# Kernel tuning notes

Measured on AMD Instinct MI355X. Metric: run time of the kernel, lower is better.

The kernel has to match this reference:

```python
import jax, jax.numpy as jnp
import numpy as np

N_GRAPHS = 256      # graphs in the batch
N_PER = 52          # nodes per peptide graph (module default num_nodes=52)
IN_CH = 21          # amino-acid one-hot features
HIDDEN = 128
OUT_EG = 128
LATENT = 64
N_LAYERS = 4


def _fc_edges(n_graphs, n_per):
    """Block-diagonal fully-connected directed edges (no self loops)."""
    base = np.arange(n_per)
    r, c = np.meshgrid(base, base, indexing='ij')
    mask = r != c
    r, c = r[mask], c[mask]                       # [n_per*(n_per-1)]
    offs = (np.arange(n_graphs) * n_per)[:, None]
    row = (r[None, :] + offs).reshape(-1)
    col = (c[None, :] + offs).reshape(-1)
    return row.astype(np.int32), col.astype(np.int32)


def setup_inputs() -> dict:
    key = jax.random.key(0)
    ks = iter(jax.random.split(key, 40))

    def rn(shape, scale=0.05):
        return jax.random.normal(next(ks), shape, dtype=jnp.float32) * scale

    N = N_GRAPHS * N_PER
    row, col = _fc_edges(N_GRAPHS, N_PER)
    L, H = N_LAYERS, HIDDEN
    return {
        'x': jax.random.normal(next(ks), (N, IN_CH), dtype=jnp.float32),
        'pos': jax.random.normal(next(ks), (N, 3), dtype=jnp.float32),
        'edge_row': jnp.asarray(row),
        'edge_col': jnp.asarray(col),
        'batch': jnp.repeat(jnp.arange(N_GRAPHS, dtype=jnp.int32), N_PER),
        'emb_in_w': rn((IN_CH, H)), 'emb_in_b': jnp.zeros((H,), jnp.float32),
        'edge_w1': rn((L, 2 * H + 1, H)), 'edge_b1': jnp.zeros((L, H), jnp.float32),
        'edge_w2': rn((L, H, H)), 'edge_b2': jnp.zeros((L, H), jnp.float32),
        'node_w1': rn((L, 2 * H, H)), 'node_b1': jnp.zeros((L, H), jnp.float32),
        'node_w2': rn((L, H, H)), 'node_b2': jnp.zeros((L, H), jnp.float32),
        'coord_w1': rn((L, H, H)), 'coord_b1': jnp.zeros((L, H), jnp.float32),
        'coord_w2': rn((L, H, 1), scale=0.001),   # xavier gain=0.001, no bias
        'emb_out_w': rn((H, OUT_EG)), 'emb_out_b': jnp.zeros((OUT_EG,), jnp.float32),
        'mean_w': rn((OUT_EG, LATENT)), 'mean_b': jnp.zeros((LATENT,), jnp.float32),
        'logvar_w': rn((OUT_EG, LATENT)), 'logvar_b': jnp.zeros((LATENT,), jnp.float32),
    }


def _segment_mean(data, ids, n):
    s = jax.ops.segment_sum(data, ids, num_segments=n)
    cnt = jax.ops.segment_sum(jnp.ones((data.shape[0],), data.dtype), ids, num_segments=n)
    return s / jnp.clip(cnt, 1.0)[:, None]


def _egcl(h, coord, row, col, p):
    """One E_GCL layer (residual=True, coords_agg='mean', no attention/tanh/normalize)."""
    ew1, eb1, ew2, eb2, nw1, nb1, nw2, nb2, cw1, cb1, cw2 = p
    n = h.shape[0]
    coord_diff = coord[row] - coord[col]                     # [E,3]
    radial = jnp.sum(coord_diff * coord_diff, axis=1, keepdims=True)  # [E,1]
    # edge model
    m = jnp.concatenate([h[row], h[col], radial], axis=1)    # [E,2H+1]
    m = jax.nn.silu(m @ ew1 + eb1)
    edge_feat = jax.nn.silu(m @ ew2 + eb2)                   # [E,H]
    # coord model: per-edge scalar, mean-aggregated onto source nodes
    t = jax.nn.silu(edge_feat @ cw1 + cb1) @ cw2             # [E,1]
    coord = coord + _segment_mean(coord_diff * t, row, n)
    # node model: sum-aggregate edge features, MLP, residual
    agg = jax.ops.segment_sum(edge_feat, row, num_segments=n)
    z = jnp.concatenate([h, agg], axis=1)                    # [N,2H]
    z = jax.nn.silu(z @ nw1 + nb1)
    h = h + (z @ nw2 + nb2)
    return h, coord


def reference(x, pos, edge_row, edge_col, batch,
              emb_in_w, emb_in_b,
              edge_w1, edge_b1, edge_w2, edge_b2,
              node_w1, node_b1, node_w2, node_b2,
              coord_w1, coord_b1, coord_w2,
              emb_out_w, emb_out_b,
              mean_w, mean_b, logvar_w, logvar_b):
    h = x @ emb_in_w + emb_in_b
    coord = pos
    for i in range(edge_w1.shape[0]):
        h, coord = _egcl(h, coord, edge_row, edge_col,
                         (edge_w1[i], edge_b1[i], edge_w2[i], edge_b2[i],
                          node_w1[i], node_b1[i], node_w2[i], node_b2[i],
                          coord_w1[i], coord_b1[i], coord_w2[i]))
    h = h @ emb_out_w + emb_out_b                            # embedding_out
    g = _segment_mean(h, batch, N_GRAPHS)                    # global_mean_pool
    mean = g @ mean_w + mean_b
    log_var = g @ logvar_w + logvar_b
    return mean, log_var
```

## Files before the change

kernel.cpp:

```cpp
#include <hip/hip_runtime.h>

constexpr int NPER = 52;
constexpr int HID  = 128;
constexpr int INCH = 21;
constexpr int NLAY = 4;
constexpr int LATD = 64;
constexpr int NGRAPH = 256;
constexpr int TPB  = 1024;
constexpr int TSTR = 424;
constexpr int TILE = 16 * TSTR;

typedef short short8 __attribute__((ext_vector_type(8)));
typedef float f32x4  __attribute__((ext_vector_type(4)));

constexpr int W1T_OFF = 0;
constexpr int W1T_SZ  = NLAY * 256 * HID;
constexpr int W2T_OFF = W1T_OFF + W1T_SZ;
constexpr int W2T_SZ  = NLAY * HID * HID;
constexpr int C1T_OFF = W2T_OFF + W2T_SZ;
constexpr int C1T_SZ  = NLAY * HID * HID;
constexpr int N1T_OFF = C1T_OFF + C1T_SZ;
constexpr int N1T_SZ  = NLAY * HID * 2 * HID;
constexpr int N2T_OFF = N1T_OFF + N1T_SZ;
constexpr int N2T_SZ  = NLAY * HID * HID;
constexpr int WS_ELEMS = N2T_OFF + N2T_SZ;

__device__ __forceinline__ unsigned cvt_pk_bf16(float a, float b) {
    unsigned r;
    asm("v_cvt_pk_bf16_f32 %0, %1, %2" : "=v"(r) : "v"(a), "v"(b));
    return r;
}
__device__ __forceinline__ unsigned short f2bf(float f) {
    return (unsigned short)cvt_pk_bf16(f, f);
}
__device__ __forceinline__ float bf2f(unsigned short h) {
    return __uint_as_float(((unsigned)h) << 16);
}
__device__ __forceinline__ float fast_rcp(float x) {
    float r;
    asm("v_rcp_f32 %0, %1" : "=v"(r) : "v"(x));
    return r;
}
__device__ __forceinline__ float silu_f(float v) {
    return v * fast_rcp(1.0f + __expf(-v));
}
__device__ __forceinline__ f32x4 mfma16(short8 a, short8 b, f32x4 c) {
    return __builtin_amdgcn_mfma_f32_16x16x32_bf16(a, b, c, 0, 0, 0);
}

__device__ __forceinline__ int tidx(int row, int e) {
    return (e >> 3) * TSTR + row * 8 + (e & 7);
}

__global__ void conv_w(const float* __restrict__ ew1, const float* __restrict__ ew2,
                       const float* __restrict__ cw1, const float* __restrict__ nw1,
                       const float* __restrict__ nw2, unsigned short* __restrict__ ws)
{
    int idx = blockIdx.x * 256 + threadIdx.x;
    if (idx >= WS_ELEMS) return;
    float v;
    if (idx < W2T_OFF) {
        int t = idx - W1T_OFF;
        int L = t / (256 * HID), rem = t % (256 * HID);
        int n = rem / HID, k = rem % HID;
        v = (n < HID) ? ew1[(size_t)L * 257 * HID + k * HID + n]
                      : ew1[(size_t)L * 257 * HID + (HID + k) * HID + (n - HID)];
    } else if (idx < C1T_OFF) {
        int t = idx - W2T_OFF;
        int L = t / (HID * HID), rem = t % (HID * HID);
        int n = rem / HID, k = rem % HID;
        v = ew2[(size_t)L * HID * HID + k * HID + n];
    } else if (idx < N1T_OFF) {
        int t = idx - C1T_OFF;
        int L = t / (HID * HID), rem = t % (HID * HID);
        int n = rem / HID, k = rem % HID;
        v = cw1[(size_t)L * HID * HID + k * HID + n];
    } else if (idx < N2T_OFF) {
        int t = idx - N1T_OFF;
        int L = t / (HID * 2 * HID), rem = t % (HID * 2 * HID);
        int n = rem / (2 * HID), k = rem % (2 * HID);
        v = nw1[(size_t)L * 2 * HID * HID + k * HID + n];
    } else {
        int t = idx - N2T_OFF;
        int L = t / (HID * HID), rem = t % (HID * HID);
        int n = rem / HID, k = rem % HID;
        v = nw2[(size_t)L * HID * HID + k * HID + n];
    }
    ws[idx] = f2bf(v);
}

constexpr int LDS_FLOATS = 1024 + 156 + 156 + 128 + 512 + 128;
constexpr size_t SHMEM_BYTES = (size_t)8 * TILE * 2 + LDS_FLOATS * 4;

__device__ __forceinline__ void coord_agg(int r, int rr, const float* tpart,
                                          const float* coord_s, float* cacc_s, int lane)
{
    float dx = 0.f, dy = 0.f, dz = 0.f;
    if (lane < NPER) {
        const float* tb = tpart + rr * 256;
        float tc = tb[lane] + tb[64 + lane] + tb[128 + lane] + tb[192 + lane];
        dx = (coord_s[r * 3 + 0] - coord_s[lane * 3 + 0]) * tc;
        dy = (coord_s[r * 3 + 1] - coord_s[lane * 3 + 1]) * tc;
        dz = (coord_s[r * 3 + 2] - coord_s[lane * 3 + 2]) * tc;
    }
    #pragma unroll
    for (int m = 1; m < 64; m <<= 1) {
        dx += __shfl_xor(dx, m); dy += __shfl_xor(dy, m); dz += __shfl_xor(dz, m);
    }
    if (lane == 0) {
        cacc_s[r * 3 + 0] = dx; cacc_s[r * 3 + 1] = dy; cacc_s[r * 3 + 2] = dz;
    }
}

extern "C" __global__ void __launch_bounds__(TPB)
egnn_mfma(const float* __restrict__ x, const float* __restrict__ pos,
          const float* __restrict__ emb_in_w, const float* __restrict__ emb_in_b,
          const float* __restrict__ edge_w1,
          const float* __restrict__ edge_b1, const float* __restrict__ edge_b2,
          const float* __restrict__ node_b1, const float* __restrict__ node_b2,
          const float* __restrict__ coord_b1, const float* __restrict__ coord_w2,
          const float* __restrict__ emb_out_w, const float* __restrict__ emb_out_b,
          const float* __restrict__ mean_w, const float* __restrict__ mean_b,
          const float* __restrict__ logvar_w, const float* __restrict__ logvar_b,
          const unsigned short* __restrict__ ws, float* __restrict__ out)
{
    extern __shared__ __align__(16) char smem[];
    unsigned short* m0_t = (unsigned short*)smem;
    unsigned short* m1_t = m0_t + TILE;
    unsigned short* e0_t = m1_t + TILE;
    unsigned short* e1_t = e0_t + TILE;
    unsigned short* h_t  = e1_t + TILE;
    unsigned short* ag_t = h_t  + TILE;
    unsigned short* A_t  = ag_t + TILE;
    unsigned short* B_t  = A_t  + TILE;
    float* aggp    = (float*)(B_t + TILE);
    float* coord_s = aggp + 1024;
    float* cacc_s  = coord_s + 156;
    float* rad_s   = cacc_s + 156;
    float* tpart   = rad_s + 128;
    float* wr_s    = tpart + 512;

    const int g    = blockIdx.x;
    const int tid  = threadIdx.x;
    const int lane = tid & 63;
    const int wv   = tid >> 6;
    const int mp   = wv >> 2;
    const int np   = wv & 3;
    const int l15  = lane & 15;
    const int kb   = lane >> 4;
    const int rowA = mp * 16 + l15;
    const int crow0 = mp * 16 + kb * 4;
    const int n0   = 32 * np + l15;
    const int n1   = n0 + 16;
    const int jp   = 2 * lane;
    const int pb   = (jp >> 3) * TSTR + (jp & 7);
    const int fo   = kb * TSTR + rowA * 8;

    {
        float* xs = (float*)m0_t;
        for (int p = tid; p < NPER * INCH; p += TPB) xs[p] = x[(size_t)g * NPER * INCH + p];
        for (int p = tid; p < NPER * 3; p += TPB)    coord_s[p] = pos[(size_t)g * NPER * 3 + p];
    }
    __syncthreads();

    for (int p = tid; p < NPER * HID; p += TPB) {
        int c = p >> 7, j = p & 127;
        float s = emb_in_b[j];
        #pragma unroll 7
        for (int k = 0; k < INCH; ++k) s += ((float*)m0_t)[c * INCH + k] * emb_in_w[k * HID + j];
        h_t[tidx(c, j)] = f2bf(s);
    }
    __syncthreads();

    for (int L = 0; L < NLAY; ++L) {
        const unsigned short* w1t = ws + W1T_OFF + (size_t)L * 256 * HID;
        const unsigned short* w2t = ws + W2T_OFF + (size_t)L * HID * HID;
        const unsigned short* c1t = ws + C1T_OFF + (size_t)L * HID * HID;
        const unsigned short* n1t = ws + N1T_OFF + (size_t)L * HID * 2 * HID;
        const unsigned short* n2t = ws + N2T_OFF + (size_t)L * HID * HID;

        short8 wE[8], wC[8];
        #pragma unroll
        for (int s = 0; s < 4; ++s) {
            wE[s]     = *(const short8*)(w2t + (size_t)n0 * HID + 32 * s + 8 * kb);
            wE[4 + s] = *(const short8*)(w2t + (size_t)n1 * HID + 32 * s + 8 * kb);
            wC[s]     = *(const short8*)(c1t + (size_t)n0 * HID + 32 * s + 8 * kb);
            wC[4 + s] = *(const short8*)(c1t + (size_t)n1 * HID + 32 * s + 8 * kb);
        }
        float eb2v[2], cb1v[2], cw2v[2];
        eb2v[0] = edge_b2[L * HID + n0];  eb2v[1] = edge_b2[L * HID + n1];
        cb1v[0] = coord_b1[L * HID + n0]; cb1v[1] = coord_b1[L * HID + n1];
        cw2v[0] = coord_w2[L * HID + n0]; cw2v[1] = coord_w2[L * HID + n1];
        if (tid < HID) wr_s[tid] = edge_w1[(size_t)L * 257 * HID + 256 * HID + tid];

        {
            f32x4 acc[4];
            #pragma unroll
            for (int q = 0; q < 4; ++q) acc[q] = (f32x4){0.f, 0.f, 0.f, 0.f};
            #pragma unroll
            for (int s = 0; s < 4; ++s) {
                short8 af = *(const short8*)(h_t + fo + s * 4 * TSTR);
                #pragma unroll
                for (int q = 0; q < 4; ++q) {
                    int n = l15 + 16 * (4 * np + q);
                    short8 bf = *(const short8*)(w1t + (size_t)n * HID + 32 * s + 8 * kb);
                    acc[q] = mfma16(af, bf, acc[q]);
                }
            }
            #pragma unroll
            for (int q = 0; q < 4; ++q) {
                int n = l15 + 16 * (4 * np + q);
                float eb1 = (n < HID) ? edge_b1[L * HID + n] : 0.f;
                #pragma unroll
                for (int reg = 0; reg < 4; ++reg) {
                    int c = crow0 + reg;
                    if (c < NPER) {
                        float v = acc[q][reg] + eb1;
                        if (n < HID) A_t[tidx(c, n)] = f2bf(v);
                        else         B_t[tidx(c, n - HID)] = f2bf(v);
                    }
                }
            }
        }
        if (tid < NPER) {
            float dx = coord_s[0] - coord_s[tid * 3 + 0];
            float dy = coord_s[1] - coord_s[tid * 3 + 1];
            float dz = coord_s[2] - coord_s[tid * 3 + 2];
            rad_s[tid] = dx * dx + dy * dy + dz * dz;
        } else if (tid >= 64 && tid < 64 + NPER) {
            int c = tid - 64;
            float dx = coord_s[3] - coord_s[c * 3 + 0];
            float dy = coord_s[4] - coord_s[c * 3 + 1];
            float dz = coord_s[5] - coord_s[c * 3 + 2];
            rad_s[64 + c] = dx * dx + dy * dy + dz * dz;
        }
        __syncthreads();

        const float wrl = wr_s[jp], wrh = wr_s[jp + 1];

        for (int gp = 0; gp < 26; ++gp) {
            const int r0 = 2 * gp, r1 = r0 + 1;

            {
                unsigned pa0 = *(const unsigned*)(A_t + pb + r0 * 8);
                unsigned pa1 = *(const unsigned*)(A_t + pb + r1 * 8);
                float A0l = bf2f((unsigned short)(pa0 & 0xffff)), A0h = bf2f((unsigned short)(pa0 >> 16));
                float A1l = bf2f((unsigned short)(pa1 & 0xffff)), A1h = bf2f((unsigned short)(pa1 >> 16));
                for (int j = wv; j < 2 * NPER; j += 16) {
                    int rr = (j >= NPER);
                    int c  = rr ? j - NPER : j;
                    float Al = rr ? A1l : A0l, Ah = rr ? A1h : A0h;
                    float rad = rad_s[rr * 64 + c];
                    unsigned bp = *(const unsigned*)(B_t + pb + c * 8);
                    float v0 = Al + bf2f((unsigned short)(bp & 0xffff)) + rad * wrl;
                    float v1 = Ah + bf2f((unsigned short)(bp >> 16))    + rad * wrh;
                    unsigned mv = cvt_pk_bf16(silu_f(v0), silu_f(v1));
                    *(unsigned*)((rr ? m1_t : m0_t) + pb + c * 8) = mv;
                }
            }
            __syncthreads();

            {
                f32x4 e00 = (f32x4){0.f,0.f,0.f,0.f}, e01 = e00, e10 = e00, e11 = e00;
                #pragma unroll
                for (int s = 0; s < 4; ++s) {
                    short8 af0 = *(const short8*)(m0_t + fo + s * 4 * TSTR);
                    short8 af1 = *(const short8*)(m1_t + fo + s * 4 * TSTR);
                    e00 = mfma16(af0, wE[s], e00); e01 = mfma16(af0, wE[4 + s], e01);
                    e10 = mfma16(af1, wE[s], e10); e11 = mfma16(af1, wE[4 + s], e11);
                }
                #pragma unroll
                for (int rr = 0; rr < 2; ++rr) {
                    f32x4 ea = rr ? e10 : e00, eb = rr ? e11 : e01;
                    unsigned short* et = rr ? e1_t : e0_t;
                    const int r = rr ? r1 : r0;
                    float a0 = 0.f, a1 = 0.f;
                    #pragma unroll
                    for (int reg = 0; reg < 4; ++reg) {
                        int c = crow0 + reg;
                        float v0 = silu_f(ea[reg] + eb2v[0]);
                        float v1 = silu_f(eb[reg] + eb2v[1]);
                        if (c < NPER) {
                            et[tidx(c, n0)] = f2bf(v0);
                            et[tidx(c, n1)] = f2bf(v1);
                            if (c != r) { a0 += v0; a1 += v1; }
                        }
                    }
                    a0 += __shfl_xor(a0, 16); a0 += __shfl_xor(a0, 32);
                    a1 += __shfl_xor(a1, 16); a1 += __shfl_xor(a1, 32);
                    if (kb == 0) {
                        float* ar = aggp + (rr * 4 + mp) * HID;
                        ar[n0] = a0; ar[n1] = a1;
                    }
                }
                if (wv < 2 && gp > 0) coord_agg(2 * gp - 2 + wv, wv, tpart, coord_s, cacc_s, lane);
            }
            __syncthreads();

            {
                f32x4 y00 = (f32x4){0.f,0.f,0.f,0.f}, y01 = y00, y10 = y00, y11 = y00;
                #pragma unroll
                for (int s = 0; s < 4; ++s) {
                    short8 af0 = *(const short8*)(e0_t + fo + s * 4 * TSTR);
                    short8 af1 = *(const short8*)(e1_t + fo + s * 4 * TSTR);
                    y00 = mfma16(af0, wC[s], y00); y01 = mfma16(af0, wC[4 + s], y01);
                    y10 = mfma16(af1, wC[s], y10); y11 = mfma16(af1, wC[4 + s], y11);
                }
                #pragma unroll
                for (int rr = 0; rr < 2; ++rr) {
                    f32x4 ya = rr ? y10 : y00, yb = rr ? y11 : y01;
                    float* tp = tpart + (rr * 4 + np) * 64;
                    #pragma unroll
                    for (int reg = 0; reg < 4; ++reg) {
                        float v = silu_f(ya[reg] + cb1v[0]) * cw2v[0]
                                + silu_f(yb[reg] + cb1v[1]) * cw2v[1];
                        v += __shfl_xor(v, 1); v += __shfl_xor(v, 2);
                        v += __shfl_xor(v, 4); v += __shfl_xor(v, 8);
                        if (l15 == 0) tp[crow0 + reg] = v;
                    }
                }
            }
            if (tid < 256) {
                int rr = tid >> 7, t = tid & 127;
                const float* ap = aggp + rr * 512;
                float a = ap[t] + ap[128 + t] + ap[256 + t] + ap[384 + t];
                ag_t[tidx(2 * gp + rr, t)] = f2bf(a);
            } else if (tid < 384 && gp + 1 < 26) {
                int t = tid - 256, rr = t >> 6, c = t & 63;
                if (c < NPER) {
                    int r = 2 * (gp + 1) + rr;
                    float dx = coord_s[r * 3 + 0] - coord_s[c * 3 + 0];
                    float dy = coord_s[r * 3 + 1] - coord_s[c * 3 + 1];
                    float dz = coord_s[r * 3 + 2] - coord_s[c * 3 + 2];
                    rad_s[rr * 64 + c] = dx * dx + dy * dy + dz * dz;
                }
            }
            __syncthreads();
        }

        if (wv < 2) coord_agg(50 + wv, wv, tpart, coord_s, cacc_s, lane);
        {
            float nb1v[2];
            nb1v[0] = node_b1[L * HID + n0]; nb1v[1] = node_b1[L * HID + n1];
            f32x4 z0 = (f32x4){0.f,0.f,0.f,0.f}, z1 = z0;
            #pragma unroll
            for (int s = 0; s < 4; ++s) {
                short8 af = *(const short8*)(h_t + fo + s * 4 * TSTR);
                z0 = mfma16(af, *(const short8*)(n1t + (size_t)n0 * 2 * HID + 32 * s + 8 * kb), z0);
                z1 = mfma16(af, *(const short8*)(n1t + (size_t)n1 * 2 * HID + 32 * s + 8 * kb), z1);
            }
            #pragma unroll
            for (int s = 0; s < 4; ++s) {
                short8 af = *(const short8*)(ag_t + fo + s * 4 * TSTR);
                z0 = mfma16(af, *(const short8*)(n1t + (size_t)n0 * 2 * HID + HID + 32 * s + 8 * kb), z0);
                z1 = mfma16(af, *(const short8*)(n1t + (size_t)n1 * 2 * HID + HID + 32 * s + 8 * kb), z1);
            }
            #pragma unroll
            for (int reg = 0; reg < 4; ++reg) {
                int c = crow0 + reg;
                if (c < NPER) {
                    m0_t[tidx(c, n0)] = f2bf(silu_f(z0[reg] + nb1v[0]));
                    m0_t[tidx(c, n1)] = f2bf(silu_f(z1[reg] + nb1v[1]));
                }
            }
        }
        __syncthreads();

        if (tid < NPER * 3) coord_s[tid] += cacc_s[tid] * (1.0f / 51.0f);
        {
            float nb2v[2];
            nb2v[0] = node_b2[L * HID + n0]; nb2v[1] = node_b2[L * HID + n1];
            f32x4 d0 = (f32x4){0.f,0.f,0.f,0.f}, d1 = d0;
            #pragma unroll
            for (int s = 0; s < 4; ++s) {
                short8 af = *(const short8*)(m0_t + fo + s * 4 * TSTR);
                d0 = mfma16(af, *(const short8*)(n2t + (size_t)n0 * HID + 32 * s + 8 * kb), d0);
                d1 = mfma16(af, *(const short8*)(n2t + (size_t)n1 * HID + 32 * s + 8 * kb), d1);
            }
            #pragma unroll
            for (int reg = 0; reg < 4; ++reg) {
                int c = crow0 + reg;
                if (c < NPER) {
                    int i0 = tidx(c, n0), i1 = tidx(c, n1);
                    h_t[i0] = f2bf(bf2f(h_t[i0]) + d0[reg] + nb2v[0]);
                    h_t[i1] = f2bf(bf2f(h_t[i1]) + d1[reg] + nb2v[1]);
                }
            }
        }
        __syncthreads();
    }

    float* gm = aggp;
    float* eg = aggp + HID;
    if (tid < HID) {
        float s = 0.f;
        for (int c = 0; c < NPER; ++c) s += bf2f(h_t[tidx(c, tid)]);
        gm[tid] = s * (1.0f / 52.0f);
    }
    __syncthreads();
    if (tid < HID) {
        float s = emb_out_b[tid];
        #pragma unroll 4
        for (int k = 0; k < HID; ++k) s += gm[k] * emb_out_w[k * HID + tid];
        eg[tid] = s;
    }
    __syncthreads();
    if (tid < 2 * LATD) {
        const int  l   = tid & (LATD - 1);
        const bool ism = tid < LATD;
        const float* W = ism ? mean_w : logvar_w;
        float s = ism ? mean_b[l] : logvar_b[l];
        #pragma unroll 4
        for (int k = 0; k < HID; ++k) s += eg[k] * W[k * LATD + l];
        out[(ism ? 0 : NGRAPH * LATD) + g * LATD + l] = s;
    }
}

extern "C" void kernel_launch(void* const* d_in, const int* in_sizes, int n_in,
                              void* d_out, int out_size, void* d_ws, size_t ws_size,
                              hipStream_t stream) {
    const float* x         = (const float*)d_in[0];
    const float* pos       = (const float*)d_in[1];
    const float* emb_in_w  = (const float*)d_in[5];
    const float* emb_in_b  = (const float*)d_in[6];
    const float* edge_w1   = (const float*)d_in[7];
    const float* edge_b1   = (const float*)d_in[8];
    const float* edge_w2   = (const float*)d_in[9];
    const float* edge_b2   = (const float*)d_in[10];
    const float* node_w1   = (const float*)d_in[11];
    const float* node_b1   = (const float*)d_in[12];
    const float* node_w2   = (const float*)d_in[13];
    const float* node_b2   = (const float*)d_in[14];
    const float* coord_w1  = (const float*)d_in[15];
    const float* coord_b1  = (const float*)d_in[16];
    const float* coord_w2  = (const float*)d_in[17];
    const float* emb_out_w = (const float*)d_in[18];
    const float* emb_out_b = (const float*)d_in[19];
    const float* mean_w    = (const float*)d_in[20];
    const float* mean_b    = (const float*)d_in[21];
    const float* logvar_w  = (const float*)d_in[22];
    const float* logvar_b  = (const float*)d_in[23];

    unsigned short* ws = (unsigned short*)d_ws;

    conv_w<<<(WS_ELEMS + 255) / 256, 256, 0, stream>>>(edge_w1, edge_w2, coord_w1,
                                                       node_w1, node_w2, ws);

    (void)hipFuncSetAttribute(reinterpret_cast<const void*>(egnn_mfma),
                              hipFuncAttributeMaxDynamicSharedMemorySize,
                              (int)SHMEM_BYTES);

    hipLaunchKernelGGL(egnn_mfma, dim3(NGRAPH), dim3(TPB), SHMEM_BYTES, stream,
                       x, pos, emb_in_w, emb_in_b, edge_w1,
                       edge_b1, edge_b2, node_b1, node_b2,
                       coord_b1, coord_w2, emb_out_w, emb_out_b,
                       mean_w, mean_b, logvar_w, logvar_b,
                       ws, (float*)d_out);
}
```

Before: 805.7 us.

## Split fused EGNN kernel into per-layer edge/node kernels with half-graph row splits

Replaces the single persistent per-graph kernel with separate launches: embedding, per-layer edge kernels split across two blocks per graph (26 rows each), per-layer node-update kernels, and a head kernel. Node features, aggregates and coordinates now round-trip through global workspace between launches. The goal is to double the block count (512 vs 256 blocks on a many-CU GPU) and cut LDS use for better occupancy, and it also reworks silu to use raw exp/rcp instructions. In exchange it adds launch overhead and extra global memory traffic.

Result: slower. 1.861 ms (+130.9%).

```diff
diff --git a/kernel.cpp b/kernel.cpp
--- a/kernel.cpp
+++ b/kernel.cpp
@@ -1,29 +1,29 @@
 #include <hip/hip_runtime.h>
 
-constexpr int NPER = 52;
-constexpr int HID  = 128;
-constexpr int INCH = 21;
-constexpr int NLAY = 4;
-constexpr int LATD = 64;
-constexpr int NGRAPH = 256;
+constexpr int NPER = 52, HID = 128, INCH = 21, NLAY = 4, LATD = 64, NGRAPH = 256;
 constexpr int TPB  = 1024;
 constexpr int TSTR = 424;
 constexpr int TILE = 16 * TSTR;
+constexpr int ASTR = 216;
+constexpr int ATILE = 16 * ASTR;
+constexpr int GSTR = 512;
+constexpr int GTILE = 16 * GSTR;
+constexpr int RHALF = 26;
+constexpr int CSTR = 160;
 
 typedef short short8 __attribute__((ext_vector_type(8)));
 typedef float f32x4  __attribute__((ext_vector_type(4)));
 
-constexpr int W1T_OFF = 0;
-constexpr int W1T_SZ  = NLAY * 256 * HID;
-constexpr int W2T_OFF = W1T_OFF + W1T_SZ;
-constexpr int W2T_SZ  = NLAY * HID * HID;
-constexpr int C1T_OFF = W2T_OFF + W2T_SZ;
-constexpr int C1T_SZ  = NLAY * HID * HID;
-constexpr int N1T_OFF = C1T_OFF + C1T_SZ;
-constexpr int N1T_SZ  = NLAY * HID * 2 * HID;
-constexpr int N2T_OFF = N1T_OFF + N1T_SZ;
-constexpr int N2T_SZ  = NLAY * HID * HID;
+constexpr int W1T_OFF = 0,                 W1T_SZ = NLAY * 256 * HID;
+constexpr int W2T_OFF = W1T_OFF + W1T_SZ,  W2T_SZ = NLAY * HID * HID;
+constexpr int C1T_OFF = W2T_OFF + W2T_SZ,  C1T_SZ = NLAY * HID * HID;
+constexpr int N1T_OFF = C1T_OFF + C1T_SZ,  N1T_SZ = NLAY * HID * 2 * HID;
+constexpr int N2T_OFF = N1T_OFF + N1T_SZ,  N2T_SZ = NLAY * HID * HID;
 constexpr int WS_ELEMS = N2T_OFF + N2T_SZ;
+constexpr int HG_OFF  = WS_ELEMS;
+constexpr int AG_OFF  = HG_OFF + NGRAPH * GTILE;
+constexpr int BF16_END = AG_OFF + NGRAPH * GTILE;
+constexpr size_t COORD_BYTE = (size_t)BF16_END * 2;
 
 __device__ __forceinline__ unsigned cvt_pk_bf16(float a, float b) {
     unsigned r;
@@ -36,20 +36,16 @@
 __device__ __forceinline__ float bf2f(unsigned short h) {
     return __uint_as_float(((unsigned)h) << 16);
 }
-__device__ __forceinline__ float fast_rcp(float x) {
-    float r;
-    asm("v_rcp_f32 %0, %1" : "=v"(r) : "v"(x));
-    return r;
-}
+__device__ __forceinline__ float blo(unsigned u) { return __uint_as_float(u << 16); }
+__device__ __forceinline__ float bhi(unsigned u) { return __uint_as_float(u & 0xffff0000u); }
 __device__ __forceinline__ float silu_f(float v) {
-    return v * fast_rcp(1.0f + __expf(-v));
+    float e, r;
+    asm("v_exp_f32 %0, %1" : "=v"(e) : "v"(v * -1.44269504088896341f));
+    asm("v_rcp_f32 %0, %1" : "=v"(r) : "v"(1.0f + e));
+    return v * r;
 }
 __device__ __forceinline__ f32x4 mfma16(short8 a, short8 b, f32x4 c) {
     return __builtin_amdgcn_mfma_f32_16x16x32_bf16(a, b, c, 0, 0, 0);
-}
-
-__device__ __forceinline__ int tidx(int row, int e) {
-    return (e >> 3) * TSTR + row * 8 + (e & 7);
 }
 
 __global__ void conv_w(const float* __restrict__ ew1, const float* __restrict__ ew2,
@@ -89,327 +85,339 @@
     ws[idx] = f2bf(v);
 }
 
-constexpr int LDS_FLOATS = 1024 + 156 + 156 + 128 + 512 + 128;
-constexpr size_t SHMEM_BYTES = (size_t)8 * TILE * 2 + LDS_FLOATS * 4;
-
-__device__ __forceinline__ void coord_agg(int r, int rr, const float* tpart,
-                                          const float* coord_s, float* cacc_s, int lane)
+__global__ void k_emb(const float* __restrict__ x, const float* __restrict__ pos,
+                      const float* __restrict__ wE, const float* __restrict__ bE,
+                      unsigned short* __restrict__ ws)
 {
-    float dx = 0.f, dy = 0.f, dz = 0.f;
-    if (lane < NPER) {
-        const float* tb = tpart + rr * 256;
-        float tc = tb[lane] + tb[64 + lane] + tb[128 + lane] + tb[192 + lane];
-        dx = (coord_s[r * 3 + 0] - coord_s[lane * 3 + 0]) * tc;
-        dy = (coord_s[r * 3 + 1] - coord_s[lane * 3 + 1]) * tc;
-        dz = (coord_s[r * 3 + 2] - coord_s[lane * 3 + 2]) * tc;
-    }
-    #pragma unroll
-    for (int m = 1; m < 64; m <<= 1) {
-        dx += __shfl_xor(dx, m); dy += __shfl_xor(dy, m); dz += __shfl_xor(dz, m);
-    }
-    if (lane == 0) {
-        cacc_s[r * 3 + 0] = dx; cacc_s[r * 3 + 1] = dy; cacc_s[r * 3 + 2] = dz;
-    }
-}
-
-extern "C" __global__ void __launch_bounds__(TPB)
-egnn_mfma(const float* __restrict__ x, const float* __restrict__ pos,
-          const float* __restrict__ emb_in_w, const float* __restrict__ emb_in_b,
-          const float* __restrict__ edge_w1,
-          const float* __restrict__ edge_b1, const float* __restrict__ edge_b2,
-          const float* __restrict__ node_b1, const float* __restrict__ node_b2,
-          const float* __restrict__ coord_b1, const float* __restrict__ coord_w2,
-          const float* __restrict__ emb_out_w, const float* __restrict__ emb_out_b,
-          const float* __restrict__ mean_w, const float* __restrict__ mean_b,
-          const float* __restrict__ logvar_w, const float* __restrict__ logvar_b,
-          const unsigned short* __restrict__ ws, float* __restrict__ out)
+    __shared__ float xs[NPER * INCH];
+    const int g = blockIdx.x, tid = threadIdx.x;
+    for (int p = tid; p < NPER * INCH; p += 256) xs[p] = x[(size_t)g * NPER * INCH + p];
+    float* coordG = (float*)((char*)ws + COORD_BYTE);
+    if (tid < NPER * 3) coordG[g * CSTR + tid] = pos[(size_t)g * NPER * 3 + tid];
+    __syncthreads();
+    unsigned short* hG = ws + HG_OFF + (size_t)g * GTILE;
+    for (int p = tid; p < NPER * HID; p += 256) {
+        int c = p >> 7, j = p & 127;
+        float s = bE[j];
+        #pragma unroll 7
+        for (int k = 0; k < INCH; ++k) s += xs[c * INCH + k] * wE[k * HID + j];
+        hG[(j >> 3) * GSTR + c * 8 + (j & 7)] = f2bf(s);
+    }
+}
+
+constexpr size_t EDGE_LDS = (size_t)(4 * TILE + ATILE) * 2
+                          + (512 + 256 + 128 + 156 + 128) * 4 + 256;
+constexpr size_t NODE_LDS = (size_t)TILE * 2 + 256;
+
+extern "C" __global__ void __launch_bounds__(TPB, 8)
+k_edge(const int L, unsigned short* __restrict__ ws,
+       const float* __restrict__ edge_w1, const float* __restrict__ edge_b1,
+       const float* __restrict__ edge_b2, const float* __restrict__ coord_b1,
+       const float* __restrict__ coord_w2)
 {
     extern __shared__ __align__(16) char smem[];
     unsigned short* m0_t = (unsigned short*)smem;
     unsigned short* m1_t = m0_t + TILE;
     unsigned short* e0_t = m1_t + TILE;
-    unsigned short* e1_t = e0_t + TILE;
-    unsigned short* h_t  = e1_t + TILE;
-    unsigned short* ag_t = h_t  + TILE;
-    unsigned short* A_t  = ag_t + TILE;
-    unsigned short* B_t  = A_t  + TILE;
-    float* aggp    = (float*)(B_t + TILE);
-    float* coord_s = aggp + 1024;
-    float* cacc_s  = coord_s + 156;
-    float* rad_s   = cacc_s + 156;
-    float* tpart   = rad_s + 128;
-    float* wr_s    = tpart + 512;
-
-    const int g    = blockIdx.x;
-    const int tid  = threadIdx.x;
-    const int lane = tid & 63;
-    const int wv   = tid >> 6;
-    const int mp   = wv >> 2;
-    const int np   = wv & 3;
-    const int l15  = lane & 15;
-    const int kb   = lane >> 4;
+    unsigned short* B_t  = e0_t + TILE;
+    unsigned short* A_t  = B_t + TILE;
+    float* aggp    = (float*)(A_t + ATILE);
+    float* tpart   = aggp + 512;
+    float* rad_s   = tpart + 256;
+    float* coord_s = rad_s + 128;
+    float* wr_s    = coord_s + 156;
+
+    const int g    = blockIdx.x >> 1;
+    const int rlo  = (blockIdx.x & 1) * RHALF;
+    const int tid  = threadIdx.x, lane = tid & 63, wv = tid >> 6;
+    const int l15  = lane & 15, kb = lane >> 4;
+    const int mp   = wv >> 2, npg = wv & 3;
     const int rowA = mp * 16 + l15;
     const int crow0 = mp * 16 + kb * 4;
-    const int n0   = 32 * np + l15;
-    const int n1   = n0 + 16;
-    const int jp   = 2 * lane;
-    const int pb   = (jp >> 3) * TSTR + (jp & 7);
+    const int n0   = npg * 32 + l15, n1 = n0 + 16;
+    const int ebA  = (n0 >> 3) * TSTR + (n0 & 7);
+    const int ebB  = (n1 >> 3) * TSTR + (n1 & 7);
     const int fo   = kb * TSTR + rowA * 8;
 
+    const unsigned short* hG = ws + HG_OFF + (size_t)g * GTILE;
+    unsigned short* agG      = ws + AG_OFF + (size_t)g * GTILE;
+    float* coordG = (float*)((char*)ws + COORD_BYTE);
+    float* caccG  = coordG + NGRAPH * CSTR;
+
+    const unsigned short* w1t = ws + W1T_OFF + (size_t)L * 256 * HID;
+    const unsigned short* w2t = ws + W2T_OFF + (size_t)L * HID * HID;
+    const unsigned short* c1t = ws + C1T_OFF + (size_t)L * HID * HID;
+
+    const float eb2v0 = edge_b2[L * HID + n0],  eb2v1 = edge_b2[L * HID + n1];
+    const float cb1v0 = coord_b1[L * HID + n0], cb1v1 = coord_b1[L * HID + n1];
+    const float cw2v0 = coord_w2[L * HID + n0], cw2v1 = coord_w2[L * HID + n1];
+
+    if (tid < NPER * 3) coord_s[tid] = coordG[g * CSTR + tid];
+    if (tid >= 256 && tid < 384)
+        wr_s[tid - 256] = edge_w1[(size_t)L * 257 * HID + 256 * HID + (tid - 256)];
+    __syncthreads();
+
     {
-        float* xs = (float*)m0_t;
-        for (int p = tid; p < NPER * INCH; p += TPB) xs[p] = x[(size_t)g * NPER * INCH + p];
-        for (int p = tid; p < NPER * 3; p += TPB)    coord_s[p] = pos[(size_t)g * NPER * 3 + p];
-    }
-    __syncthreads();
-
-    for (int p = tid; p < NPER * HID; p += TPB) {
-        int c = p >> 7, j = p & 127;
-        float s = emb_in_b[j];
-        #pragma unroll 7
-        for (int k = 0; k < INCH; ++k) s += ((float*)m0_t)[c * INCH + k] * emb_in_w[k * HID + j];
-        h_t[tidx(c, j)] = f2bf(s);
-    }
-    __syncthreads();
-
-    for (int L = 0; L < NLAY; ++L) {
-        const unsigned short* w1t = ws + W1T_OFF + (size_t)L * 256 * HID;
-        const unsigned short* w2t = ws + W2T_OFF + (size_t)L * HID * HID;
-        const unsigned short* c1t = ws + C1T_OFF + (size_t)L * HID * HID;
-        const unsigned short* n1t = ws + N1T_OFF + (size_t)L * HID * 2 * HID;
-        const unsigned short* n2t = ws + N2T_OFF + (size_t)L * HID * HID;
-
-        short8 wE[8], wC[8];
+        f32x4 acc[4];
+        #pragma unroll
+        for (int q = 0; q < 4; ++q) acc[q] = (f32x4){0.f, 0.f, 0.f, 0.f};
         #pragma unroll
         for (int s = 0; s < 4; ++s) {
-            wE[s]     = *(const short8*)(w2t + (size_t)n0 * HID + 32 * s + 8 * kb);
-            wE[4 + s] = *(const short8*)(w2t + (size_t)n1 * HID + 32 * s + 8 * kb);
-            wC[s]     = *(const short8*)(c1t + (size_t)n0 * HID + 32 * s + 8 * kb);
-            wC[4 + s] = *(const short8*)(c1t + (size_t)n1 * HID + 32 * s + 8 * kb);
-        }
-        float eb2v[2], cb1v[2], cw2v[2];
-        eb2v[0] = edge_b2[L * HID + n0];  eb2v[1] = edge_b2[L * HID + n1];
-        cb1v[0] = coord_b1[L * HID + n0]; cb1v[1] = coord_b1[L * HID + n1];
-        cw2v[0] = coord_w2[L * HID + n0]; cw2v[1] = coord_w2[L * HID + n1];
-        if (tid < HID) wr_s[tid] = edge_w1[(size_t)L * 257 * HID + 256 * HID + tid];
-
-        {
-            f32x4 acc[4];
-            #pragma unroll
-            for (int q = 0; q < 4; ++q) acc[q] = (f32x4){0.f, 0.f, 0.f, 0.f};
-            #pragma unroll
-            for (int s = 0; s < 4; ++s) {
-                short8 af = *(const short8*)(h_t + fo + s * 4 * TSTR);
-                #pragma unroll
-                for (int q = 0; q < 4; ++q) {
-                    int n = l15 + 16 * (4 * np + q);
-                    short8 bf = *(const short8*)(w1t + (size_t)n * HID + 32 * s + 8 * kb);
-                    acc[q] = mfma16(af, bf, acc[q]);
-                }
-            }
+            short8 af = *(const short8*)(hG + (4 * s + kb) * GSTR + rowA * 8);
             #pragma unroll
             for (int q = 0; q < 4; ++q) {
-                int n = l15 + 16 * (4 * np + q);
-                float eb1 = (n < HID) ? edge_b1[L * HID + n] : 0.f;
-                #pragma unroll
-                for (int reg = 0; reg < 4; ++reg) {
-                    int c = crow0 + reg;
-                    if (c < NPER) {
-                        float v = acc[q][reg] + eb1;
-                        if (n < HID) A_t[tidx(c, n)] = f2bf(v);
-                        else         B_t[tidx(c, n - HID)] = f2bf(v);
-                    }
-                }
-            }
-        }
-        if (tid < NPER) {
-            float dx = coord_s[0] - coord_s[tid * 3 + 0];
-            float dy = coord_s[1] - coord_s[tid * 3 + 1];
-            float dz = coord_s[2] - coord_s[tid * 3 + 2];
-            rad_s[tid] = dx * dx + dy * dy + dz * dz;
-        } else if (tid >= 64 && tid < 64 + NPER) {
-            int c = tid - 64;
-            float dx = coord_s[3] - coord_s[c * 3 + 0];
-            float dy = coord_s[4] - coord_s[c * 3 + 1];
-            float dz = coord_s[5] - coord_s[c * 3 + 2];
-            rad_s[64 + c] = dx * dx + dy * dy + dz * dz;
-        }
-        __syncthreads();
-
-        const float wrl = wr_s[jp], wrh = wr_s[jp + 1];
-
-        for (int gp = 0; gp < 26; ++gp) {
-            const int r0 = 2 * gp, r1 = r0 + 1;
-
-            {
-                unsigned pa0 = *(const unsigned*)(A_t + pb + r0 * 8);
-                unsigned pa1 = *(const unsigned*)(A_t + pb + r1 * 8);
-                float A0l = bf2f((unsigned short)(pa0 & 0xffff)), A0h = bf2f((unsigned short)(pa0 >> 16));
-                float A1l = bf2f((unsigned short)(pa1 & 0xffff)), A1h = bf2f((unsigned short)(pa1 >> 16));
-                for (int j = wv; j < 2 * NPER; j += 16) {
-                    int rr = (j >= NPER);
-                    int c  = rr ? j - NPER : j;
-                    float Al = rr ? A1l : A0l, Ah = rr ? A1h : A0h;
-                    float rad = rad_s[rr * 64 + c];
-                    unsigned bp = *(const unsigned*)(B_t + pb + c * 8);
-                    float v0 = Al + bf2f((unsigned short)(bp & 0xffff)) + rad * wrl;
-                    float v1 = Ah + bf2f((unsigned short)(bp >> 16))    + rad * wrh;
-                    unsigned mv = cvt_pk_bf16(silu_f(v0), silu_f(v1));
-                    *(unsigned*)((rr ? m1_t : m0_t) + pb + c * 8) = mv;
-                }
-            }
-            __syncthreads();
-
-            {
-                f32x4 e00 = (f32x4){0.f,0.f,0.f,0.f}, e01 = e00, e10 = e00, e11 = e00;
-                #pragma unroll
-                for (int s = 0; s < 4; ++s) {
-                    short8 af0 = *(const short8*)(m0_t + fo + s * 4 * TSTR);
-                    short8 af1 = *(const short8*)(m1_t + fo + s * 4 * TSTR);
-                    e00 = mfma16(af0, wE[s], e00); e01 = mfma16(af0, wE[4 + s], e01);
-                    e10 = mfma16(af1, wE[s], e10); e11 = mfma16(af1, wE[4 + s], e11);
-                }
-                #pragma unroll
-                for (int rr = 0; rr < 2; ++rr) {
-                    f32x4 ea = rr ? e10 : e00, eb = rr ? e11 : e01;
-                    unsigned short* et = rr ? e1_t : e0_t;
-                    const int r = rr ? r1 : r0;
-                    float a0 = 0.f, a1 = 0.f;
-                    #pragma unroll
-                    for (int reg = 0; reg < 4; ++reg) {
-                        int c = crow0 + reg;
-                        float v0 = silu_f(ea[reg] + eb2v[0]);
-                        float v1 = silu_f(eb[reg] + eb2v[1]);
-                        if (c < NPER) {
-                            et[tidx(c, n0)] = f2bf(v0);
-                            et[tidx(c, n1)] = f2bf(v1);
-                            if (c != r) { a0 += v0; a1 += v1; }
-                        }
-                    }
-                    a0 += __shfl_xor(a0, 16); a0 += __shfl_xor(a0, 32);
-                    a1 += __shfl_xor(a1, 16); a1 += __shfl_xor(a1, 32);
-                    if (kb == 0) {
-                        float* ar = aggp + (rr * 4 + mp) * HID;
-                        ar[n0] = a0; ar[n1] = a1;
-                    }
-                }
-                if (wv < 2 && gp > 0) coord_agg(2 * gp - 2 + wv, wv, tpart, coord_s, cacc_s, lane);
-            }
-            __syncthreads();
-
-            {
-                f32x4 y00 = (f32x4){0.f,0.f,0.f,0.f}, y01 = y00, y10 = y00, y11 = y00;
-                #pragma unroll
-                for (int s = 0; s < 4; ++s) {
-                    short8 af0 = *(const short8*)(e0_t + fo + s * 4 * TSTR);
-                    short8 af1 = *(const short8*)(e1_t + fo + s * 4 * TSTR);
-                    y00 = mfma16(af0, wC[s], y00); y01 = mfma16(af0, wC[4 + s], y01);
-                    y10 = mfma16(af1, wC[s], y10); y11 = mfma16(af1, wC[4 + s], y11);
-                }
-                #pragma unroll
-                for (int rr = 0; rr < 2; ++rr) {
-                    f32x4 ya = rr ? y10 : y00, yb = rr ? y11 : y01;
-                    float* tp = tpart + (rr * 4 + np) * 64;
-                    #pragma unroll
-                    for (int reg = 0; reg < 4; ++reg) {
-                        float v = silu_f(ya[reg] + cb1v[0]) * cw2v[0]
-                                + silu_f(yb[reg] + cb1v[1]) * cw2v[1];
-                        v += __shfl_xor(v, 1); v += __shfl_xor(v, 2);
-                        v += __shfl_xor(v, 4); v += __shfl_xor(v, 8);
-                        if (l15 == 0) tp[crow0 + reg] = v;
-                    }
-                }
-            }
-            if (tid < 256) {
-                int rr = tid >> 7, t = tid & 127;
-                const float* ap = aggp + rr * 512;
-                float a = ap[t] + ap[128 + t] + ap[256 + t] + ap[384 + t];
-                ag_t[tidx(2 * gp + rr, t)] = f2bf(a);
-            } else if (tid < 384 && gp + 1 < 26) {
-                int t = tid - 256, rr = t >> 6, c = t & 63;
-                if (c < NPER) {
-                    int r = 2 * (gp + 1) + rr;
-                    float dx = coord_s[r * 3 + 0] - coord_s[c * 3 + 0];
-                    float dy = coord_s[r * 3 + 1] - coord_s[c * 3 + 1];
-                    float dz = coord_s[r * 3 + 2] - coord_s[c * 3 + 2];
-                    rad_s[rr * 64 + c] = dx * dx + dy * dy + dz * dz;
-                }
-            }
-            __syncthreads();
-        }
-
-        if (wv < 2) coord_agg(50 + wv, wv, tpart, coord_s, cacc_s, lane);
-        {
-            float nb1v[2];
-            nb1v[0] = node_b1[L * HID + n0]; nb1v[1] = node_b1[L * HID + n1];
-            f32x4 z0 = (f32x4){0.f,0.f,0.f,0.f}, z1 = z0;
-            #pragma unroll
-            for (int s = 0; s < 4; ++s) {
-                short8 af = *(const short8*)(h_t + fo + s * 4 * TSTR);
-                z0 = mfma16(af, *(const short8*)(n1t + (size_t)n0 * 2 * HID + 32 * s + 8 * kb), z0);
-                z1 = mfma16(af, *(const short8*)(n1t + (size_t)n1 * 2 * HID + 32 * s + 8 * kb), z1);
-            }
-            #pragma unroll
-            for (int s = 0; s < 4; ++s) {
-                short8 af = *(const short8*)(ag_t + fo + s * 4 * TSTR);
-                z0 = mfma16(af, *(const short8*)(n1t + (size_t)n0 * 2 * HID + HID + 32 * s + 8 * kb), z0);
-                z1 = mfma16(af, *(const short8*)(n1t + (size_t)n1 * 2 * HID + HID + 32 * s + 8 * kb), z1);
-            }
+                int n = l15 + 16 * (4 * npg + q);
+                short8 bf = *(const short8*)(w1t + (size_t)n * HID + 32 * s + 8 * kb);
+                acc[q] = mfma16(af, bf, acc[q]);
+            }
+        }
+        #pragma unroll
+        for (int q = 0; q < 4; ++q) {
+            int n = l15 + 16 * (4 * npg + q);
+            float eb1 = (n < HID) ? edge_b1[L * HID + n] : 0.f;
             #pragma unroll
             for (int reg = 0; reg < 4; ++reg) {
                 int c = crow0 + reg;
                 if (c < NPER) {
-                    m0_t[tidx(c, n0)] = f2bf(silu_f(z0[reg] + nb1v[0]));
-                    m0_t[tidx(c, n1)] = f2bf(silu_f(z1[reg] + nb1v[1]));
+                    float v = acc[q][reg] + eb1;
+                    if (n < HID) {
+                        if (c >= rlo && c < rlo + RHALF)
+                            A_t[(n >> 3) * ASTR + (c - rlo) * 8 + (n & 7)] = f2bf(v);
+                    } else {
+                        B_t[((n - HID) >> 3) * TSTR + c * 8 + ((n - HID) & 7)] = f2bf(v);
+                    }
                 }
             }
         }
-        __syncthreads();
-
-        if (tid < NPER * 3) coord_s[tid] += cacc_s[tid] * (1.0f / 51.0f);
+        if ((wv == 14 || wv == 15) && lane < NPER) {
+            int r = rlo + (wv - 14);
+            float dx = coord_s[r * 3 + 0] - coord_s[lane * 3 + 0];
+            float dy = coord_s[r * 3 + 1] - coord_s[lane * 3 + 1];
+            float dz = coord_s[r * 3 + 2] - coord_s[lane * 3 + 2];
+            rad_s[(r & 1) * 64 + lane] = dx * dx + dy * dy + dz * dz;
+        }
+    }
+    __syncthreads();
+
+    const int mrow0 = tid >> 5;
+    const int mrow1 = mrow0 + 32;
+    const int c4  = (tid & 31) * 4;
+    const int pbB = (c4 >> 3) * TSTR + (c4 & 7);
+    const int pbA = (c4 >> 3) * ASTR + (c4 & 7);
+    float w4x, w4y, w4z, w4w;
+    { float4 t4 = *(const float4*)(wr_s + c4); w4x = t4.x; w4y = t4.y; w4z = t4.z; w4w = t4.w; }
+    float Bf0[4] = {0.f, 0.f, 0.f, 0.f}, Bf1[4] = {0.f, 0.f, 0.f, 0.f};
+    {
+        uint2 b = *(const uint2*)(B_t + pbB + mrow0 * 8);
+        Bf0[0] = blo(b.x); Bf0[1] = bhi(b.x); Bf0[2] = blo(b.y); Bf0[3] = bhi(b.y);
+    }
+    if (mrow1 < NPER) {
+        uint2 b = *(const uint2*)(B_t + pbB + mrow1 * 8);
+        Bf1[0] = blo(b.x); Bf1[1] = bhi(b.x); Bf1[2] = blo(b.y); Bf1[3] = bhi(b.y);
+    }
+
+    auto mstep = [&](int rn) {
+        unsigned short* mt = (rn & 1) ? m1_t : m0_t;
+        uint2 a = *(const uint2*)(A_t + pbA + (rn - rlo) * 8);
+        float A0 = blo(a.x), A1 = bhi(a.x), A2 = blo(a.y), A3 = bhi(a.y);
+        const float* radp = rad_s + (rn & 1) * 64;
         {
-            float nb2v[2];
-            nb2v[0] = node_b2[L * HID + n0]; nb2v[1] = node_b2[L * HID + n1];
-            f32x4 d0 = (f32x4){0.f,0.f,0.f,0.f}, d1 = d0;
+            float rad = radp[mrow0];
+            uint2 o;
+            o.x = cvt_pk_bf16(silu_f(A0 + Bf0[0] + rad * w4x), silu_f(A1 + Bf0[1] + rad * w4y));
+            o.y = cvt_pk_bf16(silu_f(A2 + Bf0[2] + rad * w4z), silu_f(A3 + Bf0[3] + rad * w4w));
+            *(uint2*)(mt + pbB + mrow0 * 8) = o;
+        }
+        if (mrow1 < NPER) {
+            float rad = radp[mrow1];
+            uint2 o;
+            o.x = cvt_pk_bf16(silu_f(A0 + Bf1[0] + rad * w4x), silu_f(A1 + Bf1[1] + rad * w4y));
+            o.y = cvt_pk_bf16(silu_f(A2 + Bf1[2] + rad * w4z), silu_f(A3 + Bf1[3] + rad * w4w));
+            *(uint2*)(mt + pbB + mrow1 * 8) = o;
+        }
+    };
+
+    auto coord_agg_f = [&](int r) {
+        float dx = 0.f, dy = 0.f, dz = 0.f;
+        if (lane < NPER) {
+            float tc = tpart[lane] + tpart[64 + lane] + tpart[128 + lane] + tpart[192 + lane];
+            dx = (coord_s[r * 3 + 0] - coord_s[lane * 3 + 0]) * tc;
+            dy = (coord_s[r * 3 + 1] - coord_s[lane * 3 + 1]) * tc;
+            dz = (coord_s[r * 3 + 2] - coord_s[lane * 3 + 2]) * tc;
+        }
+        #pragma unroll
+        for (int m = 1; m < 64; m <<= 1) {
+            dx += __shfl_xor(dx, m); dy += __shfl_xor(dy, m); dz += __shfl_xor(dz, m);
+        }
+        if (lane == 0) {
+            caccG[g * CSTR + r * 3 + 0] = dx;
+            caccG[g * CSTR + r * 3 + 1] = dy;
+            caccG[g * CSTR + r * 3 + 2] = dz;
+        }
+    };
+
+    mstep(rlo);
+    __syncthreads();
+
+    for (int ri = 0; ri < RHALF; ++ri) {
+        const int r = rlo + ri;
+        const unsigned short* mcur = (r & 1) ? m1_t : m0_t;
+
+        {
+            f32x4 ea = (f32x4){0.f, 0.f, 0.f, 0.f}, eb = ea;
             #pragma unroll
             for (int s = 0; s < 4; ++s) {
-                short8 af = *(const short8*)(m0_t + fo + s * 4 * TSTR);
-                d0 = mfma16(af, *(const short8*)(n2t + (size_t)n0 * HID + 32 * s + 8 * kb), d0);
-                d1 = mfma16(af, *(const short8*)(n2t + (size_t)n1 * HID + 32 * s + 8 * kb), d1);
-            }
+                short8 af = *(const short8*)(mcur + fo + s * 4 * TSTR);
+                ea = mfma16(af, *(const short8*)(w2t + (size_t)n0 * HID + 32 * s + 8 * kb), ea);
+                eb = mfma16(af, *(const short8*)(w2t + (size_t)n1 * HID + 32 * s + 8 * kb), eb);
+            }
+            float a0 = 0.f, a1 = 0.f;
             #pragma unroll
             for (int reg = 0; reg < 4; ++reg) {
                 int c = crow0 + reg;
+                float v0 = silu_f(ea[reg] + eb2v0);
+                float v1 = silu_f(eb[reg] + eb2v1);
                 if (c < NPER) {
-                    int i0 = tidx(c, n0), i1 = tidx(c, n1);
-                    h_t[i0] = f2bf(bf2f(h_t[i0]) + d0[reg] + nb2v[0]);
-                    h_t[i1] = f2bf(bf2f(h_t[i1]) + d1[reg] + nb2v[1]);
+                    e0_t[ebA + c * 8] = f2bf(v0);
+                    e0_t[ebB + c * 8] = f2bf(v1);
+                    if (c != r) { a0 += v0; a1 += v1; }
                 }
             }
-        }
+            a0 += __shfl_xor(a0, 16); a0 += __shfl_xor(a0, 32);
+            a1 += __shfl_xor(a1, 16); a1 += __shfl_xor(a1, 32);
+            if (kb == 0) { aggp[mp * HID + n0] = a0; aggp[mp * HID + n1] = a1; }
+        }
+        if (wv == 0 && ri > 0) coord_agg_f(r - 1);
+        if (ri + 1 < RHALF) mstep(r + 1);
         __syncthreads();
-    }
-
-    float* gm = aggp;
-    float* eg = aggp + HID;
-    if (tid < HID) {
+
+        {
+            f32x4 ya = (f32x4){0.f, 0.f, 0.f, 0.f}, yb = ya;
+            #pragma unroll
+            for (int s = 0; s < 4; ++s) {
+                short8 af = *(const short8*)(e0_t + fo + s * 4 * TSTR);
+                ya = mfma16(af, *(const short8*)(c1t + (size_t)n0 * HID + 32 * s + 8 * kb), ya);
+                yb = mfma16(af, *(const short8*)(c1t + (size_t)n1 * HID + 32 * s + 8 * kb), yb);
+            }
+            #pragma unroll
+            for (int reg = 0; reg < 4; ++reg) {
+                float v = silu_f(ya[reg] + cb1v0) * cw2v0 + silu_f(yb[reg] + cb1v1) * cw2v1;
+                v += __shfl_xor(v, 1); v += __shfl_xor(v, 2);
+                v += __shfl_xor(v, 4); v += __shfl_xor(v, 8);
+                if (l15 == 0) tpart[npg * 64 + crow0 + reg] = v;
+            }
+        }
+        if (wv == 12 || wv == 13) {
+            int t = (wv - 12) * 64 + lane;
+            float a = aggp[t] + aggp[128 + t] + aggp[256 + t] + aggp[384 + t];
+            agG[(t >> 3) * GSTR + r * 8 + (t & 7)] = f2bf(a);
+        } else if (wv == 14 && ri + 2 < RHALF && lane < NPER) {
+            int rn = r + 2;
+            float dx = coord_s[rn * 3 + 0] - coord_s[lane * 3 + 0];
+            float dy = coord_s[rn * 3 + 1] - coord_s[lane * 3 + 1];
+            float dz = coord_s[rn * 3 + 2] - coord_s[lane * 3 + 2];
+            rad_s[(rn & 1) * 64 + lane] = dx * dx + dy * dy + dz * dz;
+        }
+        __syncthreads();
+    }
+    if (wv == 0) coord_agg_f(rlo + RHALF - 1);
+}
+
+extern "C" __global__ void __launch_bounds__(TPB)
+k_node(const int L, unsigned short* __restrict__ ws,
+       const float* __restrict__ node_b1, const float* __restrict__ node_b2)
+{
+    extern __shared__ __align__(16) char smem[];
+    unsigned short* z_t = (unsigned short*)smem;
+    const int g = blockIdx.x, tid = threadIdx.x, lane = tid & 63, wv = tid >> 6;
+    const int l15 = lane & 15, kb = lane >> 4;
+    const int mp = wv >> 2, npg = wv & 3;
+    const int rowA = mp * 16 + l15, crow0 = mp * 16 + kb * 4;
+    const int n0 = npg * 32 + l15, n1 = n0 + 16;
+    const int fo = kb * TSTR + rowA * 8;
+
+    unsigned short* hG       = ws + HG_OFF + (size_t)g * GTILE;
+    const unsigned short* agG = ws + AG_OFF + (size_t)g * GTILE;
+    float* coordG = (float*)((char*)ws + COORD_BYTE);
+    float* caccG  = coordG + NGRAPH * CSTR;
+    const unsigned short* n1t = ws + N1T_OFF + (size_t)L * HID * 2 * HID;
+    const unsigned short* n2t = ws + N2T_OFF + (size_t)L * HID * HID;
+
+    if (tid < NPER * 3) coordG[g * CSTR + tid] += caccG[g * CSTR + tid] * (1.0f / 51.0f);
+
+    const float nb1v0 = node_b1[L * HID + n0], nb1v1 = node_b1[L * HID + n1];
+    const float nb2v0 = node_b2[L * HID + n0], nb2v1 = node_b2[L * HID + n1];
+
+    f32x4 z0 = (f32x4){0.f, 0.f, 0.f, 0.f}, z1 = z0;
+    #pragma unroll
+    for (int s = 0; s < 4; ++s) {
+        short8 af = *(const short8*)(hG + (4 * s + kb) * GSTR + rowA * 8);
+        z0 = mfma16(af, *(const short8*)(n1t + (size_t)n0 * 2 * HID + 32 * s + 8 * kb), z0);
+        z1 = mfma16(af, *(const short8*)(n1t + (size_t)n1 * 2 * HID + 32 * s + 8 * kb), z1);
+    }
+    #pragma unroll
+    for (int s = 0; s < 4; ++s) {
+        short8 af = *(const short8*)(agG + (4 * s + kb) * GSTR + rowA * 8);
+        z0 = mfma16(af, *(const short8*)(n1t + (size_t)n0 * 2 * HID + HID + 32 * s + 8 * kb), z0);
+        z1 = mfma16(af, *(const short8*)(n1t + (size_t)n1 * 2 * HID + HID + 32 * s + 8 * kb), z1);
+    }
+    #pragma unroll
+    for (int reg = 0; reg < 4; ++reg) {
+        int c = crow0 + reg;
+        if (c < NPER) {
+            z_t[(n0 >> 3) * TSTR + c * 8 + (n0 & 7)] = f2bf(silu_f(z0[reg] + nb1v0));
+            z_t[(n1 >> 3) * TSTR + c * 8 + (n1 & 7)] = f2bf(silu_f(z1[reg] + nb1v1));
+        }
+    }
+    __syncthreads();
+
+    f32x4 d0 = (f32x4){0.f, 0.f, 0.f, 0.f}, d1 = d0;
+    #pragma unroll
+    for (int s = 0; s < 4; ++s) {
+        short8 af = *(const short8*)(z_t + fo + s * 4 * TSTR);
+        d0 = mfma16(af, *(const short8*)(n2t + (size_t)n0 * HID + 32 * s + 8 * kb), d0);
+        d1 = mfma16(af, *(const short8*)(n2t + (size_t)n1 * HID + 32 * s + 8 * kb), d1);
+    }
+    #pragma unroll
+    for (int reg = 0; reg < 4; ++reg) {
+        int c = crow0 + reg;
+        if (c < NPER) {
+            int i0 = (n0 >> 3) * GSTR + c * 8 + (n0 & 7);
+            int i1 = (n1 >> 3) * GSTR + c * 8 + (n1 & 7);
+            hG[i0] = f2bf(bf2f(hG[i0]) + d0[reg] + nb2v0);
+            hG[i1] = f2bf(bf2f(hG[i1]) + d1[reg] + nb2v1);
+        }
+    }
+}
+
+__global__ void k_head(const unsigned short* __restrict__ ws,
+                       const float* __restrict__ eW, const float* __restrict__ eB,
+                       const float* __restrict__ mW, const float* __restrict__ mB,
+                       const float* __restrict__ lW, const float* __restrict__ lB,
+                       float* __restrict__ out)
+{
+    __shared__ float gm[HID], eg[HID];
+    const int g = blockIdx.x, tid = threadIdx.x;
+    const unsigned short* hG = ws + HG_OFF + (size_t)g * GTILE;
+    {
         float s = 0.f;
-        for (int c = 0; c < NPER; ++c) s += bf2f(h_t[tidx(c, tid)]);
+        int base = (tid >> 3) * GSTR + (tid & 7);
+        for (int c = 0; c < NPER; ++c) s += bf2f(hG[base + c * 8]);
         gm[tid] = s * (1.0f / 52.0f);
     }
     __syncthreads();
-    if (tid < HID) {
-        float s = emb_out_b[tid];
+    {
+        float s = eB[tid];
         #pragma unroll 4
-        for (int k = 0; k < HID; ++k) s += gm[k] * emb_out_w[k * HID + tid];
+        for (int k = 0; k < HID; ++k) s += gm[k] * eW[k * HID + tid];
         eg[tid] = s;
     }
     __syncthreads();
-    if (tid < 2 * LATD) {
+    {
         const int  l   = tid & (LATD - 1);
         const bool ism = tid < LATD;
-        const float* W = ism ? mean_w : logvar_w;
-        float s = ism ? mean_b[l] : logvar_b[l];
+        const float* W = ism ? mW : lW;
+        float s = ism ? mB[l] : lB[l];
         #pragma unroll 4
         for (int k = 0; k < HID; ++k) s += eg[k] * W[k * LATD + l];
         out[(ism ? 0 : NGRAPH * LATD) + g * LATD + l] = s;
@@ -441,19 +449,22 @@
     const float* logvar_w  = (const float*)d_in[22];
     const float* logvar_b  = (const float*)d_in[23];
 
-    unsigned short* ws = (unsigned short*)d_ws;
+    unsigned short* wsu = (unsigned short*)d_ws;
 
     conv_w<<<(WS_ELEMS + 255) / 256, 256, 0, stream>>>(edge_w1, edge_w2, coord_w1,
-                                                       node_w1, node_w2, ws);
-
-    (void)hipFuncSetAttribute(reinterpret_cast<const void*>(egnn_mfma),
-                              hipFuncAttributeMaxDynamicSharedMemorySize,
-                              (int)SHMEM_BYTES);
-
-    hipLaunchKernelGGL(egnn_mfma, dim3(NGRAPH), dim3(TPB), SHMEM_BYTES, stream,
-                       x, pos, emb_in_w, emb_in_b, edge_w1,
-                       edge_b1, edge_b2, node_b1, node_b2,
-                       coord_b1, coord_w2, emb_out_w, emb_out_b,
-                       mean_w, mean_b, logvar_w, logvar_b,
-                       ws, (float*)d_out);
-}
+                                                       node_w1, node_w2, wsu);
+    k_emb<<<NGRAPH, 256, 0, stream>>>(x, pos, emb_in_w, emb_in_b, wsu);
+
+    (void)hipFuncSetAttribute(reinterpret_cast<const void*>(k_edge),
+                              hipFuncAttributeMaxDynamicSharedMemorySize, (int)EDGE_LDS);
+    (void)hipFuncSetAttribute(reinterpret_cast<const void*>(k_node),
+                              hipFuncAttributeMaxDynamicSharedMemorySize, (int)NODE_LDS);
+
+    for (int L = 0; L < NLAY; ++L) {
+        k_edge<<<NGRAPH * 2, TPB, EDGE_LDS, stream>>>(L, wsu, edge_w1, edge_b1,
+                                                      edge_b2, coord_b1, coord_w2);
+        k_node<<<NGRAPH, TPB, NODE_LDS, stream>>>(L, wsu, node_b1, node_b2);
+    }
+    k_head<<<NGRAPH, 128, 0, stream>>>(wsu, emb_out_w, emb_out_b,
+                                       mean_w, mean_b, logvar_w, logvar_b, (float*)d_out);
+}
```
